# Kernel optimization log

Hardware: AMD Instinct MI355X
Metric: run time of the kernel (lower is better)

Reference implementation:

```python
import jax, jax.numpy as jnp
import numpy as np

GRID = 7
NB = 2            # boxes per cell
NC = 20           # classes
IS = NB * 4       # start of confidence channels
D = NB * 5 + NC   # 30 channels per cell
B = 8192
L_BOX = 5.0       # threshold_box
L_NEG = 0.5       # threshold_conf_neg


def _bce(logits, target):
    # stable binary_cross_entropy_with_logits, elementwise (reduction handled by caller)
    return jnp.maximum(logits, 0.0) - logits * target + jnp.log1p(jnp.exp(-jnp.abs(logits)))


def _ltrb(xywh):
    xy, wh = xywh[..., :2], xywh[..., 2:4]
    return jnp.concatenate([xy - wh * 0.5, xy + wh * 0.5], axis=-1)


def _iou(a, b):
    lt = jnp.maximum(a[..., :2], b[..., :2])
    rb = jnp.minimum(a[..., 2:], b[..., 2:])
    wh = jnp.maximum(rb - lt, 0.0)
    inter = wh[..., 0] * wh[..., 1]
    area_a = (a[..., 2] - a[..., 0]) * (a[..., 3] - a[..., 1])
    area_b = (b[..., 2] - b[..., 0]) * (b[..., 3] - b[..., 1])
    return inter / (area_a + area_b - inter + 1e-7)


def _box_loss(pb, gb):
    # (x,y) MSE + (sqrt|w|, sqrt h) MSE, summed over the 4 coords -> shape = pb.shape[:-1]
    lxy = jnp.sum((pb[..., :2] - gb[..., :2]) ** 2, axis=-1)
    lwh = jnp.sum((jnp.sqrt(jnp.abs(pb[..., 2:4])) - jnp.sqrt(gb[..., 2:4])) ** 2, axis=-1)
    return lxy + lwh


def _forward(p, g):
    batch = p.shape[0]
    conf_g = g[..., IS]                    # [B,S,S] first gt confidence
    mask_pos = conf_g > 0
    mask_neg = conf_g == 0

    # positive-cell class loss (BCE with logits, sum)
    cls_cell = _bce(p[..., NB * 5:], g[..., NB * 5:]).sum(-1)
    loss_cls_pos = jnp.sum(jnp.where(mask_pos, cls_cell, 0.0))

    # negative-cell confidence loss vs zeros
    neg_cell = _bce(p[..., IS:IS + 2], 0.0).sum(-1)
    loss_conf_neg = jnp.sum(jnp.where(mask_neg, neg_cell, 0.0))

    # per-cell boxes: [B,S,S,NB,4]
    pbox = p[..., :IS].reshape(batch, GRID, GRID, NB, 4)
    gbox = g[..., :IS].reshape(batch, GRID, GRID, NB, 4)
    poff = jnp.concatenate([jax.nn.sigmoid(pbox[..., :2]), pbox[..., 2:]], axis=-1)

    # grid offsets: colrow_index = [col=ds2, row=ds1]; xy = (offxy + colrow) / grid
    row = jnp.broadcast_to(jnp.arange(GRID, dtype=p.dtype)[:, None], (GRID, GRID))
    col = jnp.broadcast_to(jnp.arange(GRID, dtype=p.dtype)[None, :], (GRID, GRID))
    cr = jnp.stack([col, row], axis=-1)[None, :, :, None, :]   # [1,S,S,1,2]

    # IoU matching is done under no_grad in the original -> stop_gradient
    poff_ng = jax.lax.stop_gradient(poff)
    p_ltrb = _ltrb(jnp.concatenate([(poff_ng[..., :2] + cr) / GRID, poff_ng[..., 2:]], -1))
    g_ltrb = _ltrb(jnp.concatenate([(gbox[..., :2] + cr) / GRID, gbox[..., 2:]], -1))
    ious = _iou(p_ltrb[..., :, None, :], g_ltrb[..., None, :, :])   # [B,S,S,NB,NB]
    ind = jnp.argmax(ious, axis=-2)                                  # best pbox per gbox, [B,S,S,NB]

    same_g = jnp.all(gbox[..., 0, :] == gbox[..., 1, :], axis=-1)
    same_ind = ind[..., 0] == ind[..., 1]

    gathered = jnp.take_along_axis(poff, ind[..., :, None], axis=-2)  # poff[ind]
    lossA = _box_loss(gathered[..., 0, :], gbox[..., 0, :])           # identical gt boxes
    lossB = _box_loss(poff, gbox).sum(-1)
    lossC = _box_loss(gathered, gbox).sum(-1)                          # distinct matches
    box_cell = jnp.where(same_g, lossA, jnp.where(same_ind, lossB, lossC))

    pconf = p[..., IS:IS + 2]
    confA = _bce(jnp.take_along_axis(pconf, ind[..., 1:2], axis=-1)[..., 0], 1.0)
    confBC = _bce(pconf, 1.0).sum(-1)
    conf_cell = jnp.where(same_g, confA, confBC)

    loss_box_pos = jnp.sum(jnp.where(mask_pos, box_cell, 0.0))
    loss_conf_pos = jnp.sum(jnp.where(mask_pos, conf_cell, 0.0))

    nb = jnp.asarray(batch, p.dtype)
    loss_box = L_BOX * loss_box_pos / nb
    loss_conf = (loss_conf_pos + L_NEG * loss_conf_neg) / nb
    loss_cls = loss_cls_pos / nb
    return loss_box + loss_conf + loss_cls


def setup_inputs() -> dict:
    key = jax.random.key(0)
    k1, k2, k3, k4 = jax.random.split(key, 4)
    p = jax.random.normal(k1, (B, GRID, GRID, D), dtype=jnp.float32)
    # both conf channels equal (mask semantics), class targets in [0,1]
    boxes = 0.05 + 0.9 * jax.random.uniform(k2, (B, GRID, GRID, IS), dtype=jnp.float32)
    conf = (jax.random.uniform(k3, (B, GRID, GRID, 1)) < 0.3).astype(jnp.float32)
    cls = jax.random.uniform(k4, (B, GRID, GRID, NC), dtype=jnp.float32)
    g = jnp.concatenate([boxes, conf, conf, cls], axis=-1)
    return {"p_yolo_ts": p, "g_yolo_ts": g}


def reference(p_yolo_ts, g_yolo_ts):
    return _forward(p_yolo_ts, g_yolo_ts)
```

## Files before the change

### kernel.cpp

```cpp
#include <hip/hip_runtime.h>
#include <math.h>

#define GRID_N 7
#define NB 2
#define NC 20
#define IS 8
#define DCH 30
#define BATCH 8192
#define NCELL (BATCH * GRID_N * GRID_N)
#define INV_GRID (1.0f / 7.0f)
#define INV_BATCH (1.0f / 8192.0f)
#define CPB 128
#define F2C 15

__device__ __forceinline__ float bce(float l, float t) {
    return fmaxf(l, 0.0f) - l * t + __logf(1.0f + __expf(-fabsf(l)));
}

__device__ __forceinline__ float box_loss(const float* pb, const float* gb) {
    float dx = pb[0] - gb[0];
    float dy = pb[1] - gb[1];
    float dw = sqrtf(fabsf(pb[2])) - sqrtf(gb[2]);
    float dh = sqrtf(fabsf(pb[3])) - sqrtf(gb[3]);
    return dx * dx + dy * dy + dw * dw + dh * dh;
}

__global__ __launch_bounds__(CPB) void yolo_loss_kernel(
        const float* __restrict__ p, const float* __restrict__ g,
        float* __restrict__ out) {
    __shared__ float2 sp2[CPB * F2C];
    __shared__ float2 sg2[CPB * F2C];

    const int t = threadIdx.x;
    const int base = blockIdx.x * CPB;

    const float2* p2 = reinterpret_cast<const float2*>(p) + (long)base * F2C;
    const float2* g2 = reinterpret_cast<const float2*>(g) + (long)base * F2C;
    #pragma unroll
    for (int i = 0; i < F2C; ++i) {
        int idx = i * CPB + t;
        sp2[idx] = p2[idx];
    }
    #pragma unroll
    for (int i = 0; i < F2C; ++i) {
        int idx = i * CPB + t;
        sg2[idx] = g2[idx];
    }
    __syncthreads();

    const int cell = base + t;
    const int ij = cell % (GRID_N * GRID_N);
    const float fi = (float)(ij / GRID_N);
    const float fj = (float)(ij % GRID_N);

    float pv[DCH], gv[DCH];
    #pragma unroll
    for (int j = 0; j < F2C; ++j) {
        float2 v = sp2[t * F2C + j];
        pv[2*j] = v.x; pv[2*j+1] = v.y;
    }
    #pragma unroll
    for (int j = 0; j < F2C; ++j) {
        float2 v = sg2[t * F2C + j];
        gv[2*j] = v.x; gv[2*j+1] = v.y;
    }

    const float conf_g = gv[IS];
    float acc = 0.0f;

    if (conf_g == 0.0f) {
        acc = 0.5f * (bce(pv[IS], 0.0f) + bce(pv[IS + 1], 0.0f));
    } else if (conf_g > 0.0f) {
        float cls = 0.0f;
        #pragma unroll
        for (int c = 0; c < NC; ++c) cls += bce(pv[NB * 5 + c], gv[NB * 5 + c]);

        float po[NB][4];
        #pragma unroll
        for (int k = 0; k < NB; ++k) {
            po[k][0] = 1.0f / (1.0f + __expf(-pv[4*k + 0]));
            po[k][1] = 1.0f / (1.0f + __expf(-pv[4*k + 1]));
            po[k][2] = pv[4*k + 2];
            po[k][3] = pv[4*k + 3];
        }

        float pl[NB][4], gl[NB][4], pa[NB], ga[NB];
        #pragma unroll
        for (int k = 0; k < NB; ++k) {
            float cx = (po[k][0] + fj) * INV_GRID;
            float cy = (po[k][1] + fi) * INV_GRID;
            float w = po[k][2], h = po[k][3];
            pl[k][0] = cx - w * 0.5f; pl[k][1] = cy - h * 0.5f;
            pl[k][2] = cx + w * 0.5f; pl[k][3] = cy + h * 0.5f;
            pa[k] = (pl[k][2] - pl[k][0]) * (pl[k][3] - pl[k][1]);
        }
        #pragma unroll
        for (int m = 0; m < NB; ++m) {
            float cx = (gv[4*m + 0] + fj) * INV_GRID;
            float cy = (gv[4*m + 1] + fi) * INV_GRID;
            float w = gv[4*m + 2], h = gv[4*m + 3];
            gl[m][0] = cx - w * 0.5f; gl[m][1] = cy - h * 0.5f;
            gl[m][2] = cx + w * 0.5f; gl[m][3] = cy + h * 0.5f;
            ga[m] = (gl[m][2] - gl[m][0]) * (gl[m][3] - gl[m][1]);
        }

        int ind[NB];
        #pragma unroll
        for (int m = 0; m < NB; ++m) {
            float iou_km[NB];
            #pragma unroll
            for (int k = 0; k < NB; ++k) {
                float ltx = fmaxf(pl[k][0], gl[m][0]);
                float lty = fmaxf(pl[k][1], gl[m][1]);
                float rbx = fminf(pl[k][2], gl[m][2]);
                float rby = fminf(pl[k][3], gl[m][3]);
                float w = fmaxf(rbx - ltx, 0.0f);
                float h = fmaxf(rby - lty, 0.0f);
                float inter = w * h;
                iou_km[k] = inter / (pa[k] + ga[m] - inter + 1e-7f);
            }
            ind[m] = (iou_km[1] > iou_km[0]) ? 1 : 0;
        }

        float gth0[4], gth1[4];
        #pragma unroll
        for (int c = 0; c < 4; ++c) {
            gth0[c] = ind[0] ? po[1][c] : po[0][c];
            gth1[c] = ind[1] ? po[1][c] : po[0][c];
        }

        bool same_g = (gv[0] == gv[4]) && (gv[1] == gv[5]) &&
                      (gv[2] == gv[6]) && (gv[3] == gv[7]);
        bool same_ind = (ind[0] == ind[1]);

        float lossA = box_loss(gth0, &gv[0]);
        float lossB = box_loss(po[0], &gv[0]) + box_loss(po[1], &gv[4]);
        float lossC = box_loss(gth0, &gv[0]) + box_loss(gth1, &gv[4]);
        float box_cell = same_g ? lossA : (same_ind ? lossB : lossC);

        float pc0 = pv[IS], pc1 = pv[IS + 1];
        float confA = bce(ind[1] ? pc1 : pc0, 1.0f);
        float confBC = bce(pc0, 1.0f) + bce(pc1, 1.0f);
        float conf_cell = same_g ? confA : confBC;

        acc = 5.0f * box_cell + conf_cell + cls;
    }

    #pragma unroll
    for (int off = 32; off > 0; off >>= 1) acc += __shfl_down(acc, off, 64);

    __shared__ float red[CPB / 64];
    const int lane = t & 63;
    const int wid = t >> 6;
    if (lane == 0) red[wid] = acc;
    __syncthreads();
    if (t == 0) {
        float s = 0.0f;
        #pragma unroll
        for (int w = 0; w < CPB / 64; ++w) s += red[w];
        atomicAdd(out, s * INV_BATCH);
    }
}

extern "C" void kernel_launch(void* const* d_in, const int* in_sizes, int n_in,
                              void* d_out, int out_size, void* d_ws, size_t ws_size,
                              hipStream_t stream) {
    const float* p = (const float*)d_in[0];
    const float* g = (const float*)d_in[1];
    float* out = (float*)d_out;

    const int grid = NCELL / CPB;
    yolo_loss_kernel<<<grid, CPB, 0, stream>>>(p, g, out);
}
```

Measured before the change: 134.1 us.

## Load cells directly from global and compute all branches branch-free

Removes the LDS staging of both inputs and the barrier, and has each thread read its own 120-byte cell with strided float2 global loads. Both the negative and positive losses are now computed for every cell and chosen with selects instead of divergent branches. The per-box losses are precomputed as a 2x2 table so each square root is taken once, and occupancy is hinted with launch bounds of 8 blocks. The trade-off is uncoalesced per-thread strided loads and extra arithmetic on negative cells, including loading all class channels for every cell.

```diff
diff --git a/kernel.cpp b/kernel.cpp
--- a/kernel.cpp
+++ b/kernel.cpp
@@ -11,140 +11,135 @@
 #define INV_GRID (1.0f / 7.0f)
 #define INV_BATCH (1.0f / 8192.0f)
 #define CPB 128
-#define F2C 15
 
 __device__ __forceinline__ float bce(float l, float t) {
     return fmaxf(l, 0.0f) - l * t + __logf(1.0f + __expf(-fabsf(l)));
 }
 
-__device__ __forceinline__ float box_loss(const float* pb, const float* gb) {
-    float dx = pb[0] - gb[0];
-    float dy = pb[1] - gb[1];
-    float dw = sqrtf(fabsf(pb[2])) - sqrtf(gb[2]);
-    float dh = sqrtf(fabsf(pb[3])) - sqrtf(gb[3]);
-    return dx * dx + dy * dy + dw * dw + dh * dh;
-}
-
-__global__ __launch_bounds__(CPB) void yolo_loss_kernel(
+__global__ __launch_bounds__(CPB, 8) void yolo_loss_kernel(
         const float* __restrict__ p, const float* __restrict__ g,
         float* __restrict__ out) {
-    __shared__ float2 sp2[CPB * F2C];
-    __shared__ float2 sg2[CPB * F2C];
+    const int t = threadIdx.x;
+    const int cell = blockIdx.x * CPB + t;
 
-    const int t = threadIdx.x;
-    const int base = blockIdx.x * CPB;
-
-    const float2* p2 = reinterpret_cast<const float2*>(p) + (long)base * F2C;
-    const float2* g2 = reinterpret_cast<const float2*>(g) + (long)base * F2C;
-    #pragma unroll
-    for (int i = 0; i < F2C; ++i) {
-        int idx = i * CPB + t;
-        sp2[idx] = p2[idx];
-    }
-    #pragma unroll
-    for (int i = 0; i < F2C; ++i) {
-        int idx = i * CPB + t;
-        sg2[idx] = g2[idx];
-    }
-    __syncthreads();
-
-    const int cell = base + t;
     const int ij = cell % (GRID_N * GRID_N);
     const float fi = (float)(ij / GRID_N);
     const float fj = (float)(ij % GRID_N);
 
-    float pv[DCH], gv[DCH];
+    const float2* p2 = reinterpret_cast<const float2*>(p) + (long)cell * (DCH / 2);
+    const float2* g2 = reinterpret_cast<const float2*>(g) + (long)cell * (DCH / 2);
+
+    float pv[10], gv[10];
     #pragma unroll
-    for (int j = 0; j < F2C; ++j) {
-        float2 v = sp2[t * F2C + j];
-        pv[2*j] = v.x; pv[2*j+1] = v.y;
+    for (int k = 0; k < 5; ++k) {
+        float2 a = p2[k];
+        pv[2*k] = a.x; pv[2*k+1] = a.y;
     }
     #pragma unroll
-    for (int j = 0; j < F2C; ++j) {
-        float2 v = sg2[t * F2C + j];
-        gv[2*j] = v.x; gv[2*j+1] = v.y;
+    for (int k = 0; k < 5; ++k) {
+        float2 a = g2[k];
+        gv[2*k] = a.x; gv[2*k+1] = a.y;
     }
 
-    const float conf_g = gv[IS];
-    float acc = 0.0f;
+    const float conf_g = gv[8];
+    const float pc0 = pv[8], pc1 = pv[9];
 
-    if (conf_g == 0.0f) {
-        acc = 0.5f * (bce(pv[IS], 0.0f) + bce(pv[IS + 1], 0.0f));
-    } else if (conf_g > 0.0f) {
-        float cls = 0.0f;
-        #pragma unroll
-        for (int c = 0; c < NC; ++c) cls += bce(pv[NB * 5 + c], gv[NB * 5 + c]);
+    const float neg_val = 0.5f * (bce(pc0, 0.0f) + bce(pc1, 0.0f));
 
-        float po[NB][4];
+    float po[NB][4];
+    #pragma unroll
+    for (int k = 0; k < NB; ++k) {
+        po[k][0] = 1.0f / (1.0f + __expf(-pv[4*k + 0]));
+        po[k][1] = 1.0f / (1.0f + __expf(-pv[4*k + 1]));
+        po[k][2] = pv[4*k + 2];
+        po[k][3] = pv[4*k + 3];
+    }
+
+    float pl[NB][4], gl[NB][4], pa[NB], ga[NB];
+    #pragma unroll
+    for (int k = 0; k < NB; ++k) {
+        float cx = (po[k][0] + fj) * INV_GRID;
+        float cy = (po[k][1] + fi) * INV_GRID;
+        float w = po[k][2], h = po[k][3];
+        pl[k][0] = cx - w * 0.5f; pl[k][1] = cy - h * 0.5f;
+        pl[k][2] = cx + w * 0.5f; pl[k][3] = cy + h * 0.5f;
+        pa[k] = (pl[k][2] - pl[k][0]) * (pl[k][3] - pl[k][1]);
+    }
+    #pragma unroll
+    for (int m = 0; m < NB; ++m) {
+        float cx = (gv[4*m + 0] + fj) * INV_GRID;
+        float cy = (gv[4*m + 1] + fi) * INV_GRID;
+        float w = gv[4*m + 2], h = gv[4*m + 3];
+        gl[m][0] = cx - w * 0.5f; gl[m][1] = cy - h * 0.5f;
+        gl[m][2] = cx + w * 0.5f; gl[m][3] = cy + h * 0.5f;
+        ga[m] = (gl[m][2] - gl[m][0]) * (gl[m][3] - gl[m][1]);
+    }
+
+    int ind[NB];
+    #pragma unroll
+    for (int m = 0; m < NB; ++m) {
+        float iou_km[NB];
         #pragma unroll
         for (int k = 0; k < NB; ++k) {
-            po[k][0] = 1.0f / (1.0f + __expf(-pv[4*k + 0]));
-            po[k][1] = 1.0f / (1.0f + __expf(-pv[4*k + 1]));
-            po[k][2] = pv[4*k + 2];
-            po[k][3] = pv[4*k + 3];
+            float ltx = fmaxf(pl[k][0], gl[m][0]);
+            float lty = fmaxf(pl[k][1], gl[m][1]);
+            float rbx = fminf(pl[k][2], gl[m][2]);
+            float rby = fminf(pl[k][3], gl[m][3]);
+            float w = fmaxf(rbx - ltx, 0.0f);
+            float h = fmaxf(rby - lty, 0.0f);
+            float inter = w * h;
+            iou_km[k] = inter / (pa[k] + ga[m] - inter + 1e-7f);
         }
+        ind[m] = (iou_km[1] > iou_km[0]) ? 1 : 0;
+    }
 
-        float pl[NB][4], gl[NB][4], pa[NB], ga[NB];
-        #pragma unroll
-        for (int k = 0; k < NB; ++k) {
-            float cx = (po[k][0] + fj) * INV_GRID;
-            float cy = (po[k][1] + fi) * INV_GRID;
-            float w = po[k][2], h = po[k][3];
-            pl[k][0] = cx - w * 0.5f; pl[k][1] = cy - h * 0.5f;
-            pl[k][2] = cx + w * 0.5f; pl[k][3] = cy + h * 0.5f;
-            pa[k] = (pl[k][2] - pl[k][0]) * (pl[k][3] - pl[k][1]);
-        }
+    float sgw[NB][2], spw[NB][2];
+    #pragma unroll
+    for (int m = 0; m < NB; ++m) {
+        sgw[m][0] = sqrtf(gv[4*m + 2]);
+        sgw[m][1] = sqrtf(gv[4*m + 3]);
+        spw[m][0] = sqrtf(fabsf(po[m][2]));
+        spw[m][1] = sqrtf(fabsf(po[m][3]));
+    }
+
+    float bl[NB][NB];
+    #pragma unroll
+    for (int k = 0; k < NB; ++k) {
         #pragma unroll
         for (int m = 0; m < NB; ++m) {
-            float cx = (gv[4*m + 0] + fj) * INV_GRID;
-            float cy = (gv[4*m + 1] + fi) * INV_GRID;
-            float w = gv[4*m + 2], h = gv[4*m + 3];
-            gl[m][0] = cx - w * 0.5f; gl[m][1] = cy - h * 0.5f;
-            gl[m][2] = cx + w * 0.5f; gl[m][3] = cy + h * 0.5f;
-            ga[m] = (gl[m][2] - gl[m][0]) * (gl[m][3] - gl[m][1]);
+            float dx = po[k][0] - gv[4*m + 0];
+            float dy = po[k][1] - gv[4*m + 1];
+            float dw = spw[k][0] - sgw[m][0];
+            float dh = spw[k][1] - sgw[m][1];
+            bl[k][m] = dx * dx + dy * dy + dw * dw + dh * dh;
         }
+    }
 
-        int ind[NB];
-        #pragma unroll
-        for (int m = 0; m < NB; ++m) {
-            float iou_km[NB];
-            #pragma unroll
-            for (int k = 0; k < NB; ++k) {
-                float ltx = fmaxf(pl[k][0], gl[m][0]);
-                float lty = fmaxf(pl[k][1], gl[m][1]);
-                float rbx = fminf(pl[k][2], gl[m][2]);
-                float rby = fminf(pl[k][3], gl[m][3]);
-                float w = fmaxf(rbx - ltx, 0.0f);
-                float h = fmaxf(rby - lty, 0.0f);
-                float inter = w * h;
-                iou_km[k] = inter / (pa[k] + ga[m] - inter + 1e-7f);
-            }
-            ind[m] = (iou_km[1] > iou_km[0]) ? 1 : 0;
-        }
+    bool same_g = (gv[0] == gv[4]) && (gv[1] == gv[5]) &&
+                  (gv[2] == gv[6]) && (gv[3] == gv[7]);
+    bool same_ind = (ind[0] == ind[1]);
 
-        float gth0[4], gth1[4];
-        #pragma unroll
-        for (int c = 0; c < 4; ++c) {
-            gth0[c] = ind[0] ? po[1][c] : po[0][c];
-            gth1[c] = ind[1] ? po[1][c] : po[0][c];
-        }
+    float lossA = bl[ind[0]][0];
+    float lossB = bl[0][0] + bl[1][1];
+    float lossC = bl[ind[0]][0] + bl[ind[1]][1];
+    float box_cell = same_g ? lossA : (same_ind ? lossB : lossC);
 
-        bool same_g = (gv[0] == gv[4]) && (gv[1] == gv[5]) &&
-                      (gv[2] == gv[6]) && (gv[3] == gv[7]);
-        bool same_ind = (ind[0] == ind[1]);
+    float confA = bce(ind[1] ? pc1 : pc0, 1.0f);
+    float confBC = bce(pc0, 1.0f) + bce(pc1, 1.0f);
+    float conf_cell = same_g ? confA : confBC;
 
-        float lossA = box_loss(gth0, &gv[0]);
-        float lossB = box_loss(po[0], &gv[0]) + box_loss(po[1], &gv[4]);
-        float lossC = box_loss(gth0, &gv[0]) + box_loss(gth1, &gv[4]);
-        float box_cell = same_g ? lossA : (same_ind ? lossB : lossC);
+    float pos_val = 5.0f * box_cell + conf_cell;
 
-        float pc0 = pv[IS], pc1 = pv[IS + 1];
-        float confA = bce(ind[1] ? pc1 : pc0, 1.0f);
-        float confBC = bce(pc0, 1.0f) + bce(pc1, 1.0f);
-        float conf_cell = same_g ? confA : confBC;
+    float cls = 0.0f;
+    #pragma unroll
+    for (int k = 5; k < DCH / 2; ++k) {
+        float2 a = p2[k];
+        float2 b = g2[k];
+        cls += bce(a.x, b.x) + bce(a.y, b.y);
+    }
 
-        acc = 5.0f * box_cell + conf_cell + cls;
-    }
+    float acc = (conf_g == 0.0f) ? neg_val
+              : ((conf_g > 0.0f) ? (pos_val + cls) : 0.0f);
 
     #pragma unroll
     for (int off = 32; off > 0; off >>= 1) acc += __shfl_down(acc, off, 64);
```

Result: slower. 146.1 us (+9.0%).
